# Optimization experiments

Hardware: AMD Instinct MI355X
Metric: run time of the kernel (lower is better)

Reference implementation:

```python
import jax, jax.numpy as jnp
import numpy as np

N = 4096  # matrix is [N, N]; all entries are nonzero 'edges' (uniform(0,1) fill)


def setup_inputs() -> dict:
    key = jax.random.key(0)
    k1, k2, k3 = jax.random.split(key, 3)
    matrix = jax.random.uniform(k1, (N, N), dtype=jnp.float32)
    drop_param = jax.random.normal(k2, (1,), dtype=jnp.float32)
    gamma = jax.random.normal(k3, (1,), dtype=jnp.float32)
    return {"matrix": matrix, "drop_param": drop_param, "gamma": gamma,
            "drop_ratio_pct": 20}


def reference(matrix, drop_param, gamma, drop_ratio_pct):
    # Flatten: every nonzero entry is an edge. With uniform fill all N*N entries
    # are edges, so num_edges is static and k is a trace-time Python int.
    v = matrix.reshape(-1)                       # [E] edge values
    num_edges = v.shape[0]
    k = (num_edges * drop_ratio_pct) // 100      # int(num_edges * drop_ratio)

    # drop_prob = sigmoid(drop_param*(1 - v) - gamma*v)  (per-edge weight)
    logits = drop_param[0] * (1.0 - v) - gamma[0] * v
    logp = jax.nn.log_sigmoid(logits)            # log of unnormalized weight

    # Weighted sampling without replacement (Efraimidis-Spirakis / Gumbel top-k):
    # taking top-k of log(p_i) + Gumbel_i samples k indices w/o replacement with
    # probability proportional to p_i (normalization is a shift, top-k invariant).
    u = jax.random.uniform(jax.random.key(42), (num_edges,), dtype=jnp.float32,
                           minval=1e-7, maxval=1.0 - 1e-7)
    gumbel = -jnp.log(-jnp.log(u))
    keys = jnp.where(v != 0, logp + gumbel, -jnp.inf)  # only real edges eligible
    _, drop_idx = jax.lax.top_k(keys, k)         # [k] sampled edge indices

    # Vectorized scatter of zeros (replaces the Python for-loop in the original)
    dropped = v.at[drop_idx].set(0.0)
    return dropped.reshape(matrix.shape)
```

## Files before the change

### kernel.cpp

```cpp
#include <hip/hip_runtime.h>
#include <hip/hip_bf16.h>
#include <stdint.h>


#define NBINS 8192
#define NBINS_SHIFT 19
#define NBS 64
#define NBSTREAM 1024
#define NB2 256
#define LIST_CAP 2097152u
#define MINI_CAP 16384u
#define LBUF_CAP 2048
#define TIES_TILE 4096
#define SLACK 3
#define MARGIN 2.0e-4f

__device__ __forceinline__ unsigned tf_bits(unsigned i) {
  const unsigned ks0 = 0u;
  const unsigned ks1 = 42u;
  const unsigned ks2 = 0x1BD11BDAu ^ 0u ^ 42u;
  unsigned x0 = 0u + ks0;
  unsigned x1 = i + ks1;
#define TF_R(rot) { x0 += x1; \
  x1 = __builtin_amdgcn_alignbit(x1, x1, 32u - (rot)); x1 ^= x0; }
  TF_R(13) TF_R(15) TF_R(26) TF_R(6)
  x0 += ks1; x1 += ks2 + 1u;
  TF_R(17) TF_R(29) TF_R(16) TF_R(24)
  x0 += ks2; x1 += ks0 + 2u;
  TF_R(13) TF_R(15) TF_R(26) TF_R(6)
  x0 += ks0; x1 += ks1 + 3u;
  TF_R(17) TF_R(29) TF_R(16) TF_R(24)
  x0 += ks1; x1 += ks2 + 4u;
  TF_R(13) TF_R(15) TF_R(26) TF_R(6)
  x0 += ks2; x1 += ks0 + 5u;
#undef TF_R
  return x0 ^ x1;
}

__device__ __forceinline__ float uniform_from_bits(unsigned bits) {
  unsigned fb = (bits >> 9) | 0x3f800000u;
  float f = __uint_as_float(fb) - 1.0f;
  const float minv = 1e-7f;
  const float maxv = __uint_as_float(0x3F7FFFFEu);
  float r = __fsub_rn(maxv, minv);
  float u = __fadd_rn(__fmul_rn(f, r), minv);
  return fmaxf(minv, u);
}

__device__ __forceinline__ float xla_expf(float input) {
  const float exp_hi = 88.3762626647950f;
  const float exp_lo = -88.3762626647949f;
  float x = fminf(fmaxf(input, exp_lo), exp_hi);
  float fx = floorf(__fadd_rn(__fmul_rn(x, 1.44269504088896341f), 0.5f));
  float tmp = __fmul_rn(0.693359375f, fx);
  float z = __fmul_rn(-2.12194440e-4f, fx);
  x = __fsub_rn(x, tmp);
  x = __fsub_rn(x, z);
  z = __fmul_rn(x, x);
  float y = __fadd_rn(__fmul_rn(x, 1.9875691500e-4f), 1.3981999507e-3f);
  y = __fadd_rn(__fmul_rn(y, x), 8.3334519073e-3f);
  y = __fadd_rn(__fmul_rn(y, x), 4.1665795894e-2f);
  y = __fadd_rn(__fmul_rn(y, x), 1.6666665459e-1f);
  y = __fadd_rn(__fmul_rn(y, x), 5.0000001201e-1f);
  y = __fadd_rn(__fmul_rn(y, z), x);
  y = __fadd_rn(1.0f, y);
  int n = (int)fx;
  float p2n = __int_as_float((n + 0x7f) << 23);
  return fmaxf(__fmul_rn(y, p2n), input);
}

__device__ __forceinline__ float xla_logf(float input) {
  float t0 = fmaxf(input, __uint_as_float(0x00800000u));
  unsigned ib = __float_as_uint(t0);
  int emm0 = (int)(ib >> 23) - 0x7f;
  float e = __fadd_rn(1.0f, (float)emm0);
  float m = __uint_as_float((ib & 0x807fffffu) | 0x3f000000u);
  bool mask = m < 0.707106781186547524f;
  float t1 = mask ? m : 0.0f;
  m = __fsub_rn(m, 1.0f);
  e = __fsub_rn(e, mask ? 1.0f : 0.0f);
  m = __fadd_rn(m, t1);
  float x2 = __fmul_rn(m, m);
  float x3 = __fmul_rn(x2, m);
  float y  = __fadd_rn(__fmul_rn(m, 7.0376836292e-2f), -1.1514610310e-1f);
  float y1 = __fadd_rn(__fmul_rn(m, -1.2420140846e-1f), 1.4249322787e-1f);
  float y2 = __fadd_rn(__fmul_rn(m, 2.0000714765e-1f), -2.4999993993e-1f);
  y  = __fadd_rn(__fmul_rn(y, m), 1.1676998740e-1f);
  y1 = __fadd_rn(__fmul_rn(y1, m), -1.6668057665e-1f);
  y2 = __fadd_rn(__fmul_rn(y2, m), 3.3333331174e-1f);
  y = __fadd_rn(__fmul_rn(y, x3), y1);
  y = __fadd_rn(__fmul_rn(y, x3), y2);
  y = __fmul_rn(y, x3);
  y = __fadd_rn(y, __fmul_rn(-2.12194440e-4f, e));
  y = __fsub_rn(y, __fmul_rn(0.5f, x2));
  m = __fadd_rn(m, y);
  m = __fadd_rn(m, __fmul_rn(0.693359375f, e));
  return m;
}

__device__ __forceinline__ float xla_log1pf(float x) {
  float for_large = xla_logf(__fadd_rn(x, 1.0f));
  float for_small = __fmul_rn(__fadd_rn(__fmul_rn(-0.5f, x), 1.0f), x);
  return (fabsf(x) < 1e-4f) ? for_small : for_large;
}

__device__ __forceinline__ unsigned encode_f(float f) {
  unsigned b = __float_as_uint(f);
  return (b & 0x80000000u) ? ~b : (b | 0x80000000u);
}
__device__ __forceinline__ float decode_f(unsigned c) {
  unsigned b = (c & 0x80000000u) ? (c ^ 0x80000000u) : ~c;
  return __uint_as_float(b);
}

__device__ __forceinline__ unsigned compute_ou(unsigned i, float v, float dp, float g) {
  if (v == 0.0f) return 0u;
  unsigned bits = tf_bits(i);
  float u = uniform_from_bits(bits);
  float lg = xla_logf(u);
  float gum = -xla_logf(-lg);
  float t = __fsub_rn(1.0f, v);
  float lx = __fsub_rn(__fmul_rn(dp, t), __fmul_rn(g, v));
  float ex = xla_expf(-fabsf(lx));
  float l1p = xla_log1pf(ex);
  float lp = -(__fadd_rn(fmaxf(-lx, 0.0f), l1p));
  float key = __fadd_rn(lp, gum);
  return encode_f(key);
}

__device__ __forceinline__ float approx_key(unsigned i, float v, float dp, float g) {
  if (v == 0.0f) return -INFINITY;
  unsigned bits = tf_bits(i);
  float u = uniform_from_bits(bits);
  float lg = __logf(u);
  float gum = -__logf(-lg);
  float t = __fsub_rn(1.0f, v);
  float lx = __fsub_rn(__fmul_rn(dp, t), __fmul_rn(g, v));
  float ex = __expf(-fabsf(lx));
  float for_small = __fmul_rn(__fadd_rn(__fmul_rn(-0.5f, ex), 1.0f), ex);
  float l1p = (fabsf(ex) < 1e-4f) ? for_small : __logf(__fadd_rn(ex, 1.0f));
  float lp = -(__fadd_rn(fmaxf(-lx, 0.0f), l1p));
  return __fadd_rn(lp, gum);
}

__device__ __forceinline__ void set_band(unsigned* state, int B, int w) {
  int plo = B - w; if (plo < 32) plo = 32;
  int phi = B + w;
  unsigned blo_c = (unsigned)plo << NBINS_SHIFT;
  float blo_v = decode_f(blo_c);
  float bhi_v; unsigned bhi_c;
  if (phi >= NBINS - 1) { bhi_v = INFINITY; bhi_c = encode_f(INFINITY); }
  else { bhi_c = (unsigned)(phi + 1) << NBINS_SHIFT; bhi_v = decode_f(bhi_c); }
  state[2] = blo_c; state[3] = bhi_c;
  state[16] = __float_as_uint(blo_v);
  state[17] = __float_as_uint(bhi_v);
  state[18] = __float_as_uint(blo_v + MARGIN);
  state[19] = __float_as_uint(bhi_v - MARGIN);
  unsigned span = bhi_c - blo_c;
  unsigned sh = 0;
  while ((span >> sh) >= 4096u) ++sh;
  state[12] = sh;
}

__global__ __launch_bounds__(1024) void sample_hist_kernel(
    const float* __restrict__ v, const float* __restrict__ dpp,
    const float* __restrict__ gp, unsigned* __restrict__ hist_s,
    int nvec, int chunk, int spb) {
  __shared__ unsigned h[NBINS];
  for (int j = threadIdx.x; j < NBINS; j += 1024) h[j] = 0;
  __syncthreads();
  float dp = dpp[0], g = gp[0];
  int t = threadIdx.x;
  if (t < spb) {
    int iv = blockIdx.x * chunk + t;
    if (iv < nvec) {
      float4 vv = reinterpret_cast<const float4*>(v)[iv];
      unsigned base = (unsigned)iv << 2;
      atomicAdd(&h[encode_f(approx_key(base + 0u, vv.x, dp, g)) >> NBINS_SHIFT], 1u);
      atomicAdd(&h[encode_f(approx_key(base + 1u, vv.y, dp, g)) >> NBINS_SHIFT], 1u);
      atomicAdd(&h[encode_f(approx_key(base + 2u, vv.z, dp, g)) >> NBINS_SHIFT], 1u);
      atomicAdd(&h[encode_f(approx_key(base + 3u, vv.w, dp, g)) >> NBINS_SHIFT], 1u);
    }
  }
  __syncthreads();
  for (int j = threadIdx.x; j < NBINS; j += 1024)
    if (h[j]) atomicAdd(&hist_s[j], h[j]);
}

__global__ __launch_bounds__(1024) void find_sample_kernel(
    const unsigned* __restrict__ hist_s, unsigned* __restrict__ state,
    const int* __restrict__ pct_p, long long Etot, long long SN) {
  __shared__ unsigned s[1024];
  __shared__ int bs_sh;
  int t = threadIdx.x;
  if (t == 0) bs_sh = NBINS / 2;
  unsigned hh[8];
  unsigned tot = 0;
  #pragma unroll
  for (int j = 0; j < 8; ++j) { hh[j] = hist_s[t * 8 + j]; tot += hh[j]; }
  s[t] = tot;
  __syncthreads();
  for (int off = 1; off < 1024; off <<= 1) {
    unsigned add = (t + off < 1024) ? s[t + off] : 0u;
    __syncthreads();
    s[t] += add;
    __syncthreads();
  }
  long long k = (Etot * (long long)pct_p[0]) / 100;
  long long ks = (Etot > 0) ? (k * SN) / Etot : 0;
  if (ks < 1) ks = 1;
  long long above_next = (t < 1023) ? (long long)s[t + 1] : 0;
  if (above_next < ks && ks <= above_next + (long long)tot) {
    long long above = above_next;
    for (int b = 7; b >= 0; --b) {
      if (above < ks && ks <= above + (long long)hh[b]) { bs_sh = t * 8 + b; break; }
      above += (long long)hh[b];
    }
  }
  __syncthreads();
  if (t == 0) {
    state[6] = (unsigned)k;
    state[0] = (unsigned)bs_sh;
    if (k == 0) {
      state[15] = 0u;
      state[2] = 0xFFFFFFFFu; state[3] = 0xFFFFFFFFu; state[12] = 0u;
      state[16] = state[17] = state[18] = state[19] = __float_as_uint(INFINITY);
    } else {
      set_band(state, bs_sh, SLACK);
    }
  }
}

__global__ __launch_bounds__(512) void stream_kernel(
    const float* __restrict__ v, const float* __restrict__ dpp,
    const float* __restrict__ gp, float* __restrict__ out,
    unsigned* __restrict__ state, uint2* __restrict__ list, int E, int mode) {
  if (mode == 1 && state[15] == 0u) return;
  __shared__ uint2 lbuf[LBUF_CAP];
  __shared__ unsigned lcnt, lbase, s_a, s_hi, s_lo;
  if (threadIdx.x == 0) { lcnt = 0; s_a = 0; s_hi = 0; s_lo = 0; }
  __syncthreads();
  float blo_v = __uint_as_float(state[16]);
  float bhi_v = __uint_as_float(state[17]);
  float clo_v = __uint_as_float(state[18]);
  float chi_v = __uint_as_float(state[19]);
  float dp = dpp[0], g = gp[0];
  int nvec = E >> 2;
  int stride = gridDim.x * 512;
  unsigned a_c = 0, hi_c = 0, lo_c = 0;
  for (int iv = blockIdx.x * 512 + threadIdx.x; iv < nvec; iv += stride) {
    float4 vv = reinterpret_cast<const float4*>(v)[iv];
    unsigned base = (unsigned)iv << 2;
    float kk[4];
    kk[0] = approx_key(base + 0u, vv.x, dp, g);
    kk[1] = approx_key(base + 1u, vv.y, dp, g);
    kk[2] = approx_key(base + 2u, vv.z, dp, g);
    kk[3] = approx_key(base + 3u, vv.w, dp, g);
    float vals[4] = {vv.x, vv.y, vv.z, vv.w};
    float res[4];
    #pragma unroll
    for (int j = 0; j < 4; ++j) {
      bool drop = kk[j] > bhi_v;
      a_c  += drop ? 1u : 0u;
      hi_c += (kk[j] >= chi_v) ? 1u : 0u;
      lo_c += (kk[j] >= clo_v) ? 1u : 0u;
      res[j] = drop ? 0.0f : vals[j];
      if (!drop && kk[j] >= blo_v) {
        unsigned p = atomicAdd(&lcnt, 1u);
        uint2 ent = make_uint2(base + (unsigned)j, __float_as_uint(vals[j]));
        if (p < LBUF_CAP) lbuf[p] = ent;
        else {
          unsigned q = atomicAdd(&state[4], 1u);
          if (q < LIST_CAP) list[q] = ent;
        }
      }
    }
    float4 oo; oo.x = res[0]; oo.y = res[1]; oo.z = res[2]; oo.w = res[3];
    reinterpret_cast<float4*>(out)[iv] = oo;
  }
  if (blockIdx.x == 0) {
    for (int i = (nvec << 2) + threadIdx.x; i < E; i += 512) {
      float val = v[i];
      float key = approx_key((unsigned)i, val, dp, g);
      bool drop = key > bhi_v;
      a_c  += drop ? 1u : 0u;
      hi_c += (key >= chi_v) ? 1u : 0u;
      lo_c += (key >= clo_v) ? 1u : 0u;
      out[i] = drop ? 0.0f : val;
      if (!drop && key >= blo_v) {
        unsigned p = atomicAdd(&lcnt, 1u);
        uint2 ent = make_uint2((unsigned)i, __float_as_uint(val));
        if (p < LBUF_CAP) lbuf[p] = ent;
        else {
          unsigned q = atomicAdd(&state[4], 1u);
          if (q < LIST_CAP) list[q] = ent;
        }
      }
    }
  }
  #pragma unroll
  for (int off = 32; off > 0; off >>= 1) {
    a_c  += __shfl_xor(a_c, off);
    hi_c += __shfl_xor(hi_c, off);
    lo_c += __shfl_xor(lo_c, off);
  }
  if ((threadIdx.x & 63) == 0) {
    if (a_c)  atomicAdd(&s_a, a_c);
    if (hi_c) atomicAdd(&s_hi, hi_c);
    if (lo_c) atomicAdd(&s_lo, lo_c);
  }
  __syncthreads();
  if (threadIdx.x == 0) {
    lbase = atomicAdd(&state[4], min(lcnt, (unsigned)LBUF_CAP));
    if (s_a)  atomicAdd(&state[5], s_a);
    if (s_hi) atomicAdd(&state[20], s_hi);
    if (s_lo) atomicAdd(&state[21], s_lo);
  }
  __syncthreads();
  unsigned n = min(lcnt, (unsigned)LBUF_CAP);
  for (unsigned j = threadIdx.x; j < n; j += 512) {
    unsigned q = lbase + j;
    if (q < LIST_CAP) list[q] = lbuf[j];
  }
}

__global__ __launch_bounds__(64) void find_verify_kernel(
    unsigned* __restrict__ state, int final_round) {
  if (threadIdx.x != 0) return;
  unsigned k = state[6];
  if (k == 0u) { state[15] = 0u; return; }
  unsigned hi = state[20], lo = state[21], M = state[4];
  bool cond_hi = hi < k;
  bool cond_lo = lo >= k;
  bool cond_M = M <= LIST_CAP;
  if ((cond_hi && cond_lo && cond_M) || final_round) { state[15] = 0u; return; }
  state[15] = 1u;
  int B = (int)state[0];
  int w = SLACK;
  if (!cond_hi)      B += 2 * SLACK - 1;
  else if (!cond_lo) B -= 2 * SLACK - 1;
  else               w = 1;
  state[0] = (unsigned)B;
  set_band(state, B, w);
  state[4] = 0u; state[5] = 0u; state[20] = 0u; state[21] = 0u;
}

__device__ __forceinline__ unsigned band_bin(unsigned ec, unsigned blo,
                                             unsigned span, unsigned sh) {
  if (ec <= blo) return 0u;
  unsigned d = ec - blo;
  if (d > span) d = span;
  return d >> sh;
}

__global__ __launch_bounds__(256) void exact_eval_kernel(
    const float* __restrict__ dpp, const float* __restrict__ gp,
    const uint2* __restrict__ list, unsigned* __restrict__ elist,
    const unsigned* __restrict__ state, unsigned* __restrict__ blockhist2) {
  __shared__ unsigned h[4096];
  for (int j = threadIdx.x; j < 4096; j += 256) h[j] = 0;
  __syncthreads();
  unsigned M = min(state[4], LIST_CAP);
  unsigned blo = state[2], span = state[3] - state[2], sh = state[12];
  float dp = dpp[0], g = gp[0];
  for (unsigned e = blockIdx.x * 256 + threadIdx.x; e < M; e += gridDim.x * 256) {
    uint2 le = list[e];
    unsigned ec = compute_ou(le.x, __uint_as_float(le.y), dp, g);
    elist[e] = ec;
    atomicAdd(&h[band_bin(ec, blo, span, sh)], 1u);
  }
  __syncthreads();
  unsigned* row = blockhist2 + (size_t)blockIdx.x * 4096;
  for (int j = threadIdx.x; j < 4096; j += 256) row[j] = h[j];
}

__global__ __launch_bounds__(256) void reduce_hist2_kernel(
    const unsigned* __restrict__ blockhist2, unsigned* __restrict__ hist2) {
  int j = blockIdx.x * 256 + threadIdx.x;
  unsigned s = 0;
  for (int b = 0; b < NB2; ++b) s += blockhist2[(size_t)b * 4096 + j];
  hist2[j] = s;
}

__global__ __launch_bounds__(1024) void find_band_kernel(
    const unsigned* __restrict__ hist2, unsigned* __restrict__ state) {
  __shared__ unsigned s[1024];
  int t = threadIdx.x;
  unsigned hh[4];
  unsigned tot = 0;
  #pragma unroll
  for (int j = 0; j < 4; ++j) { hh[j] = hist2[t * 4 + j]; tot += hh[j]; }
  s[t] = tot;
  __syncthreads();
  for (int off = 1; off < 1024; off <<= 1) {
    unsigned add = (t + off < 1024) ? s[t + off] : 0u;
    __syncthreads();
    s[t] += add;
    __syncthreads();
  }
  unsigned kp = state[6] - state[5];
  if (kp == 0u || kp > s[0]) {
    if (t == 0) { state[7] = 0xFFFFFFFFu; state[8] = 0u; }
    return;
  }
  unsigned above_next = (t < 1023) ? s[t + 1] : 0u;
  if (above_next < kp && kp <= s[t]) {
    unsigned above = above_next;
    for (int b = 3; b >= 0; --b) {
      if (above < kp && kp <= above + hh[b]) {
        state[7] = (unsigned)(t * 4 + b);
        state[8] = kp - above;
        break;
      }
      above += hh[b];
    }
  }
}

__global__ __launch_bounds__(256) void band_drop_kernel(
    const uint2* __restrict__ list, const unsigned* __restrict__ elist,
    unsigned* __restrict__ state, float* __restrict__ out,
    uint2* __restrict__ mini) {
  unsigned M = min(state[4], LIST_CAP);
  unsigned Eb = state[7];
  unsigned blo = state[2], span = state[3] - state[2], sh = state[12];
  for (unsigned e = blockIdx.x * 256 + threadIdx.x; e < M; e += gridDim.x * 256) {
    unsigned ec = elist[e];
    unsigned bin = band_bin(ec, blo, span, sh);
    if (bin > Eb) out[list[e].x] = 0.0f;
    else if (bin == Eb) {
      unsigned q = atomicAdd(&state[11], 1u);
      if (q < MINI_CAP) mini[q] = make_uint2(ec, list[e].x);
    }
  }
}

__global__ __launch_bounds__(1024) void mini_ties_kernel(
    const uint2* __restrict__ mini, const unsigned* __restrict__ state,
    float* __restrict__ out) {
  __shared__ uint2 tile[TIES_TILE];
  unsigned m = min(state[11], MINI_CAP);
  unsigned r = state[8];
  if (r == 0u || m == 0u) return;
  int tid = threadIdx.x;
  for (unsigned e0 = 0; e0 < m; e0 += blockDim.x) {
    unsigned e = e0 + tid;
    bool valid = e < m;
    unsigned my_ec = 0, my_idx = 0;
    if (valid) { uint2 me = mini[e]; my_ec = me.x; my_idx = me.y; }
    unsigned rank = 0;
    for (unsigned t0 = 0; t0 < m; t0 += TIES_TILE) {
      unsigned tn = min((unsigned)TIES_TILE, m - t0);
      __syncthreads();
      for (unsigned j = tid; j < tn; j += blockDim.x) tile[j] = mini[t0 + j];
      __syncthreads();
      if (valid) {
        for (unsigned j = 0; j < tn; ++j) {
          uint2 o = tile[j];
          rank += (o.x > my_ec || (o.x == my_ec && o.y < my_idx)) ? 1u : 0u;
        }
      }
    }
    if (valid && rank < r) out[my_idx] = 0.0f;
  }
}

extern "C" void kernel_launch(void* const* d_in, const int* in_sizes, int n_in,
                              void* d_out, int out_size, void* d_ws, size_t ws_size,
                              hipStream_t stream) {
  const float* v  = (const float*)d_in[0];
  const float* dp = (const float*)d_in[1];
  const float* g  = (const float*)d_in[2];
  const int* pct  = (const int*)d_in[3];
  float* out = (float*)d_out;
  int E = in_sizes[0];

  uint8_t* ws = (uint8_t*)d_ws;
  const size_t STATE_OFF = 0;
  const size_t HISTS_OFF = 4 * 1024;
  const size_t HIST2_OFF = 64 * 1024;
  const size_t MINI_OFF  = 128 * 1024;
  const size_t BH2_OFF   = (size_t)1 << 20;
  const size_t LIST_OFF  = (size_t)5 << 20;
  const size_t ELIST_OFF = (size_t)21 << 20;
  const size_t NEED = ELIST_OFF + (size_t)LIST_CAP * 4;

  if (ws_size < NEED) {
    hipMemcpyAsync(out, v, (size_t)E * 4, hipMemcpyDeviceToDevice, stream);
    return;
  }

  unsigned* state  = (unsigned*)(ws + STATE_OFF);
  unsigned* hist_s = (unsigned*)(ws + HISTS_OFF);
  unsigned* hist2  = (unsigned*)(ws + HIST2_OFF);
  uint2*    mini   = (uint2*)(ws + MINI_OFF);
  unsigned* bh2    = (unsigned*)(ws + BH2_OFF);
  uint2*    list   = (uint2*)(ws + LIST_OFF);
  unsigned* elist  = (unsigned*)(ws + ELIST_OFF);

  int nvec = E >> 2;
  int chunk = (nvec + NBS - 1) / NBS;
  int spb = chunk < 1024 ? chunk : 1024;
  long long SN = (long long)NBS * (long long)spb * 4;

  hipMemsetAsync(ws, 0, 40 * 1024, stream);

  sample_hist_kernel<<<NBS, 1024, 0, stream>>>(v, dp, g, hist_s, nvec, chunk, spb);
  find_sample_kernel<<<1, 1024, 0, stream>>>(hist_s, state, pct, (long long)E, SN);
  stream_kernel<<<NBSTREAM, 512, 0, stream>>>(v, dp, g, out, state, list, E, 0);
  find_verify_kernel<<<1, 64, 0, stream>>>(state, 0);
  stream_kernel<<<NBSTREAM, 512, 0, stream>>>(v, dp, g, out, state, list, E, 1);
  find_verify_kernel<<<1, 64, 0, stream>>>(state, 1);
  exact_eval_kernel<<<NB2, 256, 0, stream>>>(dp, g, list, elist, state, bh2);
  reduce_hist2_kernel<<<16, 256, 0, stream>>>(bh2, hist2);
  find_band_kernel<<<1, 1024, 0, stream>>>(hist2, state);
  band_drop_kernel<<<256, 256, 0, stream>>>(list, elist, state, out, mini);
  mini_ties_kernel<<<1, 1024, 0, stream>>>(mini, state, out);
}
```

Before: 131.3 us.

## Compare exponentiated thresholds against Gumbel weights using a sigmoid lookup table

The streaming pass no longer builds each full key (log-sigmoid plus Gumbel, two logs and an exp per element). It rewrites the test key > t as -log(u) < sigmoid(logit) * exp(-t). Per-band constants exp(-t) are precomputed in set_band, and sigmoid comes from a per-block shared-memory table with linear interpolation. This is meant to cut transcendental work in the dominant memory-plus-compute pass. The old key path is kept as a fallback when the constants overflow. Other changes: the second verify launch is dropped, the exact-eval grid is doubled, and workspace offsets move. The interpolated sigmoid only approximates the exact value near band edges, so correctness relies on the margins and the later exact evaluation.

```diff
diff --git a/kernel.cpp b/kernel.cpp
--- a/kernel.cpp
+++ b/kernel.cpp
@@ -7,7 +7,8 @@
 #define NBINS_SHIFT 19
 #define NBS 64
 #define NBSTREAM 1024
-#define NB2 256
+#define NB2 512
+#define LUTN 2048
 #define LIST_CAP 2097152u
 #define MINI_CAP 16384u
 #define LBUF_CAP 2048
@@ -151,11 +152,22 @@
   float bhi_v; unsigned bhi_c;
   if (phi >= NBINS - 1) { bhi_v = INFINITY; bhi_c = encode_f(INFINITY); }
   else { bhi_c = (unsigned)(phi + 1) << NBINS_SHIFT; bhi_v = decode_f(bhi_c); }
+  float clo_v = blo_v + MARGIN;
+  float chi_v = bhi_v - MARGIN;
   state[2] = blo_c; state[3] = bhi_c;
   state[16] = __float_as_uint(blo_v);
   state[17] = __float_as_uint(bhi_v);
-  state[18] = __float_as_uint(blo_v + MARGIN);
-  state[19] = __float_as_uint(bhi_v - MARGIN);
+  state[18] = __float_as_uint(clo_v);
+  state[19] = __float_as_uint(chi_v);
+  float Cb = __expf(-blo_v);
+  float Cl = __expf(-clo_v);
+  float Ch = (chi_v == INFINITY) ? 0.0f : __expf(-chi_v);
+  float Cd = (bhi_v == INFINITY) ? 0.0f : __expf(-bhi_v);
+  state[23] = __float_as_uint(Cb);
+  state[24] = __float_as_uint(Cd);
+  state[25] = __float_as_uint(Cl);
+  state[26] = __float_as_uint(Ch);
+  state[22] = (isfinite(Cb) && isfinite(Cl)) ? 0u : 1u;
   unsigned span = bhi_c - blo_c;
   unsigned sh = 0;
   while ((span >> sh) >= 4096u) ++sh;
@@ -222,9 +234,10 @@
     state[6] = (unsigned)k;
     state[0] = (unsigned)bs_sh;
     if (k == 0) {
-      state[15] = 0u;
+      state[15] = 0u; state[22] = 0u;
       state[2] = 0xFFFFFFFFu; state[3] = 0xFFFFFFFFu; state[12] = 0u;
       state[16] = state[17] = state[18] = state[19] = __float_as_uint(INFINITY);
+      state[23] = state[24] = state[25] = state[26] = 0u;
     } else {
       set_band(state, bs_sh, SLACK);
     }
@@ -236,49 +249,104 @@
     const float* __restrict__ gp, float* __restrict__ out,
     unsigned* __restrict__ state, uint2* __restrict__ list, int E, int mode) {
   if (mode == 1 && state[15] == 0u) return;
+  __shared__ float lut[LUTN + 1];
   __shared__ uint2 lbuf[LBUF_CAP];
   __shared__ unsigned lcnt, lbase, s_a, s_hi, s_lo;
   if (threadIdx.x == 0) { lcnt = 0; s_a = 0; s_hi = 0; s_lo = 0; }
-  __syncthreads();
-  float blo_v = __uint_as_float(state[16]);
-  float bhi_v = __uint_as_float(state[17]);
-  float clo_v = __uint_as_float(state[18]);
-  float chi_v = __uint_as_float(state[19]);
   float dp = dpp[0], g = gp[0];
+  for (int j = threadIdx.x; j <= LUTN; j += 512) {
+    float vv = (float)j * (1.0f / (float)LUTN);
+    float lx = __fsub_rn(__fmul_rn(dp, 1.0f - vv), __fmul_rn(g, vv));
+    lut[j] = 1.0f / (1.0f + __expf(-lx));
+  }
+  __syncthreads();
   int nvec = E >> 2;
   int stride = gridDim.x * 512;
   unsigned a_c = 0, hi_c = 0, lo_c = 0;
-  for (int iv = blockIdx.x * 512 + threadIdx.x; iv < nvec; iv += stride) {
-    float4 vv = reinterpret_cast<const float4*>(v)[iv];
-    unsigned base = (unsigned)iv << 2;
-    float kk[4];
-    kk[0] = approx_key(base + 0u, vv.x, dp, g);
-    kk[1] = approx_key(base + 1u, vv.y, dp, g);
-    kk[2] = approx_key(base + 2u, vv.z, dp, g);
-    kk[3] = approx_key(base + 3u, vv.w, dp, g);
-    float vals[4] = {vv.x, vv.y, vv.z, vv.w};
-    float res[4];
-    #pragma unroll
-    for (int j = 0; j < 4; ++j) {
-      bool drop = kk[j] > bhi_v;
-      a_c  += drop ? 1u : 0u;
-      hi_c += (kk[j] >= chi_v) ? 1u : 0u;
-      lo_c += (kk[j] >= clo_v) ? 1u : 0u;
-      res[j] = drop ? 0.0f : vals[j];
-      if (!drop && kk[j] >= blo_v) {
-        unsigned p = atomicAdd(&lcnt, 1u);
-        uint2 ent = make_uint2(base + (unsigned)j, __float_as_uint(vals[j]));
-        if (p < LBUF_CAP) lbuf[p] = ent;
-        else {
-          unsigned q = atomicAdd(&state[4], 1u);
-          if (q < LIST_CAP) list[q] = ent;
+
+  if (state[22] == 0u) {
+    float Cb = __uint_as_float(state[23]);
+    float Cd = __uint_as_float(state[24]);
+    float Cl = __uint_as_float(state[25]);
+    float Ch = __uint_as_float(state[26]);
+    for (int iv = blockIdx.x * 512 + threadIdx.x; iv < nvec; iv += stride) {
+      float4 vv = reinterpret_cast<const float4*>(v)[iv];
+      unsigned base = (unsigned)iv << 2;
+      float vals[4] = {vv.x, vv.y, vv.z, vv.w};
+      float w[4], P[4];
+      #pragma unroll
+      for (int j = 0; j < 4; ++j) {
+        unsigned bits = tf_bits(base + (unsigned)j);
+        float u = uniform_from_bits(bits);
+        float wv = -__logf(u);
+        w[j] = (vals[j] == 0.0f) ? INFINITY : wv;
+        float tp = vals[j] * (float)LUTN;
+        int ii = (int)tp;
+        ii = min(ii, LUTN - 1);
+        float fr = tp - (float)ii;
+        float p0 = lut[ii], p1 = lut[ii + 1];
+        P[j] = __fmaf_rn(fr, p1 - p0, p0);
+      }
+      float res[4];
+      #pragma unroll
+      for (int j = 0; j < 4; ++j) {
+        bool drop = w[j] < P[j] * Cd;
+        a_c  += drop ? 1u : 0u;
+        hi_c += (w[j] <= P[j] * Ch) ? 1u : 0u;
+        lo_c += (w[j] <= P[j] * Cl) ? 1u : 0u;
+        res[j] = drop ? 0.0f : vals[j];
+        if (!drop && w[j] <= P[j] * Cb) {
+          unsigned p = atomicAdd(&lcnt, 1u);
+          uint2 ent = make_uint2(base + (unsigned)j, __float_as_uint(vals[j]));
+          if (p < LBUF_CAP) lbuf[p] = ent;
+          else {
+            unsigned q = atomicAdd(&state[4], 1u);
+            if (q < LIST_CAP) list[q] = ent;
+          }
         }
       }
-    }
-    float4 oo; oo.x = res[0]; oo.y = res[1]; oo.z = res[2]; oo.w = res[3];
-    reinterpret_cast<float4*>(out)[iv] = oo;
+      float4 oo; oo.x = res[0]; oo.y = res[1]; oo.z = res[2]; oo.w = res[3];
+      reinterpret_cast<float4*>(out)[iv] = oo;
+    }
+  } else {
+    float blo_v = __uint_as_float(state[16]);
+    float bhi_v = __uint_as_float(state[17]);
+    float clo_v = __uint_as_float(state[18]);
+    float chi_v = __uint_as_float(state[19]);
+    for (int iv = blockIdx.x * 512 + threadIdx.x; iv < nvec; iv += stride) {
+      float4 vv = reinterpret_cast<const float4*>(v)[iv];
+      unsigned base = (unsigned)iv << 2;
+      float vals[4] = {vv.x, vv.y, vv.z, vv.w};
+      float kk[4];
+      #pragma unroll
+      for (int j = 0; j < 4; ++j) kk[j] = approx_key(base + (unsigned)j, vals[j], dp, g);
+      float res[4];
+      #pragma unroll
+      for (int j = 0; j < 4; ++j) {
+        bool drop = kk[j] > bhi_v;
+        a_c  += drop ? 1u : 0u;
+        hi_c += (kk[j] >= chi_v) ? 1u : 0u;
+        lo_c += (kk[j] >= clo_v) ? 1u : 0u;
+        res[j] = drop ? 0.0f : vals[j];
+        if (!drop && kk[j] >= blo_v) {
+          unsigned p = atomicAdd(&lcnt, 1u);
+          uint2 ent = make_uint2(base + (unsigned)j, __float_as_uint(vals[j]));
+          if (p < LBUF_CAP) lbuf[p] = ent;
+          else {
+            unsigned q = atomicAdd(&state[4], 1u);
+            if (q < LIST_CAP) list[q] = ent;
+          }
+        }
+      }
+      float4 oo; oo.x = res[0]; oo.y = res[1]; oo.z = res[2]; oo.w = res[3];
+      reinterpret_cast<float4*>(out)[iv] = oo;
+    }
   }
   if (blockIdx.x == 0) {
+    float blo_v = __uint_as_float(state[16]);
+    float bhi_v = __uint_as_float(state[17]);
+    float clo_v = __uint_as_float(state[18]);
+    float chi_v = __uint_as_float(state[19]);
     for (int i = (nvec << 2) + threadIdx.x; i < E; i += 512) {
       float val = v[i];
       float key = approx_key((unsigned)i, val, dp, g);
@@ -325,7 +393,7 @@
 }
 
 __global__ __launch_bounds__(64) void find_verify_kernel(
-    unsigned* __restrict__ state, int final_round) {
+    unsigned* __restrict__ state) {
   if (threadIdx.x != 0) return;
   unsigned k = state[6];
   if (k == 0u) { state[15] = 0u; return; }
@@ -333,7 +401,7 @@
   bool cond_hi = hi < k;
   bool cond_lo = lo >= k;
   bool cond_M = M <= LIST_CAP;
-  if ((cond_hi && cond_lo && cond_M) || final_round) { state[15] = 0u; return; }
+  if (cond_hi && cond_lo && cond_M) { state[15] = 0u; return; }
   state[15] = 1u;
   int B = (int)state[0];
   int w = SLACK;
@@ -481,8 +549,8 @@
   const size_t HIST2_OFF = 64 * 1024;
   const size_t MINI_OFF  = 128 * 1024;
   const size_t BH2_OFF   = (size_t)1 << 20;
-  const size_t LIST_OFF  = (size_t)5 << 20;
-  const size_t ELIST_OFF = (size_t)21 << 20;
+  const size_t LIST_OFF  = (size_t)9 << 20;
+  const size_t ELIST_OFF = (size_t)25 << 20;
   const size_t NEED = ELIST_OFF + (size_t)LIST_CAP * 4;
 
   if (ws_size < NEED) {
@@ -508,9 +576,8 @@
   sample_hist_kernel<<<NBS, 1024, 0, stream>>>(v, dp, g, hist_s, nvec, chunk, spb);
   find_sample_kernel<<<1, 1024, 0, stream>>>(hist_s, state, pct, (long long)E, SN);
   stream_kernel<<<NBSTREAM, 512, 0, stream>>>(v, dp, g, out, state, list, E, 0);
-  find_verify_kernel<<<1, 64, 0, stream>>>(state, 0);
+  find_verify_kernel<<<1, 64, 0, stream>>>(state);
   stream_kernel<<<NBSTREAM, 512, 0, stream>>>(v, dp, g, out, state, list, E, 1);
-  find_verify_kernel<<<1, 64, 0, stream>>>(state, 1);
   exact_eval_kernel<<<NB2, 256, 0, stream>>>(dp, g, list, elist, state, bh2);
   reduce_hist2_kernel<<<16, 256, 0, stream>>>(bh2, hist2);
   find_band_kernel<<<1, 1024, 0, stream>>>(hist2, state);
```

New measurement: 129.6 us. Within noise of the previous version (-1.3%).
